# Optimization experiments

Measured on AMD Instinct MI355X. Metric: run time of the kernel, lower is better.

Reference implementation:

```python
import jax, jax.numpy as jnp
import numpy as np

B, N, C, H = 4, 2048, 768, 12
D = C // H  # 64
EPS = 1e-12


def setup_inputs() -> dict:
    key = jax.random.key(0)
    ks = jax.random.split(key, 8)
    s = 0.02
    return {
        "x": jax.random.normal(ks[0], (B, N, C), dtype=jnp.float32),
        "Wq": jax.random.normal(ks[1], (C, C), dtype=jnp.float32) * s,
        "bq": jnp.zeros((C,), dtype=jnp.float32),
        "Wkv": jax.random.normal(ks[2], (C, 2 * C), dtype=jnp.float32) * s,
        "bkv": jnp.zeros((2 * C,), dtype=jnp.float32),
        "Wproj": jax.random.normal(ks[3], (C, C), dtype=jnp.float32) * s,
        "bproj": jnp.zeros((C,), dtype=jnp.float32),
        "scale": jnp.full((1, H, 1, 1), D ** -0.5, dtype=jnp.float32),
    }


def _l2norm(t):
    # F.normalize(dim=-1): x / max(||x||_2, eps)
    n = jnp.sqrt(jnp.sum(t * t, axis=-1, keepdims=True))
    return t / jnp.maximum(n, EPS)


def reference(x, Wq, bq, Wkv, bkv, Wproj, bproj, scale):
    b, n, c = x.shape
    q = (x @ Wq + bq).reshape(b, n, H, D).transpose(0, 2, 1, 3)        # [B,H,N,D]
    kv = (x @ Wkv + bkv).reshape(b, n, 2, H, D).transpose(2, 0, 3, 1, 4)
    k, v = kv[0], kv[1]                                                # [B,H,N,D]
    q = _l2norm(q)
    k = _l2norm(k)
    attn = jnp.einsum("bhqd,bhkd->bhqk", q, k) * scale                 # [B,H,N,N]
    attn = jax.nn.softmax(attn, axis=-1)
    out = jnp.einsum("bhqk,bhkd->bhqd", attn, v)                       # [B,H,N,D]
    out = out.transpose(0, 2, 1, 3).reshape(b, n, c)
    return out @ Wproj + bproj
```

## Files before the change

### kernel.cpp

```cpp
#include <hip/hip_runtime.h>
#include <hip/hip_bf16.h>
#include <math.h>


typedef short bf16x8 __attribute__((ext_vector_type(8)));
typedef float f32x4 __attribute__((ext_vector_type(4)));
typedef float f32x16 __attribute__((ext_vector_type(16)));

static __device__ __forceinline__ unsigned short f2bf(float f) {
    unsigned int u = __float_as_uint(f);
    unsigned int r = u + 0x7fff + ((u >> 16) & 1);
    return (unsigned short)(r >> 16);
}
static __device__ __forceinline__ unsigned int pack2(float a, float b) {
    return (unsigned int)f2bf(a) | ((unsigned int)f2bf(b) << 16);
}
static __device__ __forceinline__ unsigned int cvtpk(float a, float b) {
    unsigned int r;
    asm("v_cvt_pk_bf16_f32 %0, %1, %2" : "=v"(r) : "v"(a), "v"(b));
    return r;
}
static __device__ __forceinline__ void gl_lds16(const void* g, void* l) {
    __builtin_amdgcn_global_load_lds(
        (const __attribute__((address_space(1))) unsigned int*)g,
        (__attribute__((address_space(3))) unsigned int*)l, 16, 0, 0);
}

__global__ __launch_bounds__(256) void convx_kernel(
    const float* __restrict__ in, unsigned short* __restrict__ out)
{
    size_t i = ((size_t)blockIdx.x * 256 + threadIdx.x) * 8;
    float4 a = *(const float4*)&in[i];
    float4 b = *(const float4*)&in[i + 4];
    uint4 o = make_uint4(pack2(a.x, a.y), pack2(a.z, a.w), pack2(b.x, b.y), pack2(b.z, b.w));
    *(uint4*)&out[i] = o;
}

__global__ __launch_bounds__(256) void convT_kernel(
    const float* __restrict__ A, int ldA, const float* __restrict__ Bs, int ldB, int split,
    unsigned short* __restrict__ out)
{
    __shared__ char tb[8192];
    const int c0 = blockIdx.x * 64, k0 = blockIdx.y * 64;
    const int t = threadIdx.x;
    const int kl = t >> 2, cq = (t & 3) * 16;
    const float* src; int ld; int cbase;
    if (c0 < split) { src = A;  ld = ldA; cbase = c0; }
    else            { src = Bs; ld = ldB; cbase = c0 - split; }
    #pragma unroll
    for (int jj = 0; jj < 4; ++jj) {
        float4 v = *(const float4*)&src[(size_t)(k0 + kl) * ld + cbase + cq + jj * 4];
        float vv[4] = {v.x, v.y, v.z, v.w};
        #pragma unroll
        for (int je = 0; je < 4; ++je) {
            int c = cq + jj * 4 + je;
            *(unsigned short*)(tb + c * 128 + ((kl * 2) ^ ((c & 7) << 4))) = f2bf(vv[je]);
        }
    }
    __syncthreads();
    const int cl = t >> 2, u2 = (t & 3) * 2;
    uint4 r0 = *(const uint4*)(tb + cl * 128 + ((u2 ^ (cl & 7)) << 4));
    uint4 r1 = *(const uint4*)(tb + cl * 128 + (((u2 + 1) ^ (cl & 7)) << 4));
    size_t ob = (size_t)(c0 + cl) * 768 + k0 + (t & 3) * 16;
    *(uint4*)&out[ob] = r0;
    *(uint4*)&out[ob + 8] = r1;
}

__global__ __launch_bounds__(256) void qkv_gemm_kernel(
    const unsigned short* __restrict__ xb, const unsigned short* __restrict__ WT,
    const float* __restrict__ bq, const float* __restrict__ bkv,
    const float* __restrict__ scale,
    unsigned short* __restrict__ Qb, unsigned short* __restrict__ Kb,
    unsigned short* __restrict__ Vtb)
{
    __shared__ char lds[32768] __attribute__((aligned(16)));

    const int ct = blockIdx.x;
    const int row0 = blockIdx.y * 128;
    const int tid = threadIdx.x;
    const int w = tid >> 6, l = tid & 63;
    const int g = l >> 4, ln = l & 15;
    const int wr = w >> 1, wc = w & 1;
    const int col0 = ct * 128;

    const int srow = (w & 1) * 64 + (l >> 3);
    const int su = ((l & 7) ^ (l >> 3)) * 16;
    const char* s = (w < 2)
        ? (const char*)xb + (size_t)(row0 + srow) * 1536 + su
        : (const char*)WT + (size_t)(col0 + srow) * 1536 + su;
    char* dbase = lds + ((w >= 2) ? 16384 : 0) + (w & 1) * 8192;

    f32x4 acc[4][4];
    #pragma unroll
    for (int m = 0; m < 4; ++m)
        #pragma unroll
        for (int n = 0; n < 4; ++n) acc[m][n] = (f32x4){0.f, 0.f, 0.f, 0.f};

    const int arow = (wr * 64 + ln) * 128;
    const int brow = 16384 + (wc * 64 + ln) * 128;
    const int x0 = ((0 + g) ^ (ln & 7)) * 16;
    const int x1 = ((4 + g) ^ (ln & 7)) * 16;

    for (int ks = 0; ks < 12; ++ks) {
        __syncthreads();
        #pragma unroll
        for (int j = 0; j < 8; ++j)
            gl_lds16(s + (size_t)j * 8 * 1536, dbase + j * 1024);
        s += 128;
        __syncthreads();
        #pragma unroll
        for (int kc = 0; kc < 2; ++kc) {
            const int xo = kc ? x1 : x0;
            bf16x8 af[4], bfr[4];
            #pragma unroll
            for (int m = 0; m < 4; ++m) af[m] = *(const bf16x8*)(lds + arow + m * 2048 + xo);
            #pragma unroll
            for (int n = 0; n < 4; ++n) bfr[n] = *(const bf16x8*)(lds + brow + n * 2048 + xo);
            #pragma unroll
            for (int m = 0; m < 4; ++m)
                #pragma unroll
                for (int n = 0; n < 4; ++n)
                    acc[m][n] = __builtin_amdgcn_mfma_f32_16x16x32_bf16(af[m], bfr[n], acc[m][n], 0, 0, 0);
        }
    }

    const int co = col0 + wc * 64 + ln;
    float bv[4];
    #pragma unroll
    for (int n = 0; n < 4; ++n) {
        int c = co + n * 16;
        bv[n] = (c < 768) ? bq[c] : bkv[c - 768];
    }
    const int region = ct / 6;
    const int h = (ct % 6) * 2 + wc;

    if (region < 2) {
        unsigned short* dst = (region == 0) ? Qb : Kb;
        const float post = (region == 0) ? scale[0] * 1.4426950408889634f : 1.0f;
        #pragma unroll
        for (int m = 0; m < 4; ++m) {
            #pragma unroll
            for (int n = 0; n < 4; ++n)
                #pragma unroll
                for (int r = 0; r < 4; ++r) acc[m][n][r] += bv[n];
            #pragma unroll
            for (int r = 0; r < 4; ++r) {
                float ss = 0.f;
                #pragma unroll
                for (int n = 0; n < 4; ++n) ss += acc[m][n][r] * acc[m][n][r];
                ss += __shfl_xor(ss, 1); ss += __shfl_xor(ss, 2);
                ss += __shfl_xor(ss, 4); ss += __shfl_xor(ss, 8);
                float inv = post / fmaxf(sqrtf(ss), 1e-12f);
                int t = row0 + wr * 64 + m * 16 + g * 4 + r;
                int b = t >> 11, nt = t & 2047;
                size_t base = ((size_t)(b * 12 + h) * 2048 + nt) * 64 + ln;
                #pragma unroll
                for (int n = 0; n < 4; ++n)
                    dst[base + n * 16] = f2bf(acc[m][n][r] * inv);
            }
        }
    } else {
        char* tb = lds + w * 8192;
        __syncthreads();
        #pragma unroll
        for (int m = 0; m < 4; ++m)
            #pragma unroll
            for (int n = 0; n < 4; ++n)
                #pragma unroll
                for (int r = 0; r < 4; ++r) {
                    int d = n * 16 + ln;
                    int tok = m * 16 + g * 4 + r;
                    *(unsigned short*)(tb + d * 128 + ((tok * 2) ^ ((d & 7) << 4))) =
                        f2bf(acc[m][n][r] + bv[n]);
                }
        __syncthreads();
        const int t0 = row0 + wr * 64;
        const int b = t0 >> 11, n0 = t0 & 2047;
        #pragma unroll
        for (int i = 0; i < 8; ++i) {
            int d = i * 8 + (l >> 3);
            uint4 v = *(const uint4*)(tb + d * 128 + (((l & 7) ^ (d & 7)) << 4));
            *(uint4*)&Vtb[((size_t)(b * 12 + h) * 64 + d) * 2048 + n0 + (l & 7) * 8] = v;
        }
    }
}

__global__ __launch_bounds__(256, 3) void attn_kernel(
    const unsigned short* __restrict__ Qg, const unsigned short* __restrict__ Kg,
    const unsigned short* __restrict__ Vtg,
    unsigned short* __restrict__ O)
{
    __shared__ char lds[32768] __attribute__((aligned(16)));

    const int bid = blockIdx.y * 16 + blockIdx.x;
    const int swzb = (bid & 7) * 96 + (bid >> 3);
    const int bh = swzb >> 4;
    const int q0 = (swzb & 15) * 128;

    const int tid = threadIdx.x;
    const int w  = tid >> 6;
    const int l  = tid & 63;
    const int lo = l & 31;
    const int hi = l >> 5;

    const int srow = w * 16 + (l >> 3);
    const int su   = ((l & 7) ^ (l >> 3)) * 16;
    const char* kS = (const char*)Kg  + ((size_t)bh * 2048 + srow) * 128 + su;
    const char* vS = (const char*)Vtg + ((size_t)bh * 64   + srow) * 4096 + su;
    char* kD = lds + w * 2048;
    char* vD = lds + 16384 + w * 2048;

    bf16x8 qf[4];
    {
        const unsigned short* qp = Qg + ((size_t)bh * 2048 + q0 + w * 32 + lo) * 64 + hi * 8;
        qf[0] = *(const bf16x8*)(qp);
        qf[1] = *(const bf16x8*)(qp + 16);
        qf[2] = *(const bf16x8*)(qp + 32);
        qf[3] = *(const bf16x8*)(qp + 48);
    }

    const int swz = (lo & 7) << 4;
    const int rowb = lo * 128;
    int coff[4];
    #pragma unroll
    for (int c = 0; c < 4; ++c) coff[c] = (c * 32 + hi * 16) ^ swz;

    f32x16 oacc0, oacc1;
    #pragma unroll
    for (int r = 0; r < 16; ++r) { oacc0[r] = 0.f; oacc1[r] = 0.f; }
    float rs = 0.f;

    const f32x16 zero16 = {0.f,0.f,0.f,0.f,0.f,0.f,0.f,0.f,0.f,0.f,0.f,0.f,0.f,0.f,0.f,0.f};

    auto compute = [&](const int OFF) {
        const char* Kb = lds + OFF;
        const char* Vb = lds + 16384 + OFF;

        f32x16 s0, s1;
        __builtin_amdgcn_s_setprio(1);
        s0 = __builtin_amdgcn_mfma_f32_32x32x16_bf16(*(const bf16x8*)(Kb + rowb + coff[0]), qf[0], zero16, 0, 0, 0);
        s0 = __builtin_amdgcn_mfma_f32_32x32x16_bf16(*(const bf16x8*)(Kb + rowb + coff[1]), qf[1], s0, 0, 0, 0);
        s0 = __builtin_amdgcn_mfma_f32_32x32x16_bf16(*(const bf16x8*)(Kb + rowb + coff[2]), qf[2], s0, 0, 0, 0);
        s0 = __builtin_amdgcn_mfma_f32_32x32x16_bf16(*(const bf16x8*)(Kb + rowb + coff[3]), qf[3], s0, 0, 0, 0);
        s1 = __builtin_amdgcn_mfma_f32_32x32x16_bf16(*(const bf16x8*)(Kb + 4096 + rowb + coff[0]), qf[0], zero16, 0, 0, 0);
        s1 = __builtin_amdgcn_mfma_f32_32x32x16_bf16(*(const bf16x8*)(Kb + 4096 + rowb + coff[1]), qf[1], s1, 0, 0, 0);
        s1 = __builtin_amdgcn_mfma_f32_32x32x16_bf16(*(const bf16x8*)(Kb + 4096 + rowb + coff[2]), qf[2], s1, 0, 0, 0);
        s1 = __builtin_amdgcn_mfma_f32_32x32x16_bf16(*(const bf16x8*)(Kb + 4096 + rowb + coff[3]), qf[3], s1, 0, 0, 0);
        __builtin_amdgcn_s_setprio(0);

        #pragma unroll
        for (int r = 0; r < 16; ++r) s0[r] = __builtin_amdgcn_exp2f(s0[r]);
        #pragma unroll
        for (int r = 0; r < 16; ++r) s1[r] = __builtin_amdgcn_exp2f(s1[r]);
        float t0 = 0.f, t1 = 0.f;
        #pragma unroll
        for (int r = 0; r < 16; ++r) { t0 += s0[r]; t1 += s1[r]; }
        rs += t0 + t1;

        #pragma unroll
        for (int kb = 0; kb < 2; ++kb) {
            const f32x16 ec = kb ? s1 : s0;
            #pragma unroll
            for (int ksb = 0; ksb < 2; ++ksb) {
                const int ks = kb * 2 + ksb;
                const int rqA = ksb * 2, rqB = rqA + 1;
                unsigned int uA0 = cvtpk(ec[rqA * 4 + 0], ec[rqA * 4 + 1]);
                unsigned int uA1 = cvtpk(ec[rqA * 4 + 2], ec[rqA * 4 + 3]);
                unsigned int uB0 = cvtpk(ec[rqB * 4 + 0], ec[rqB * 4 + 1]);
                unsigned int uB1 = cvtpk(ec[rqB * 4 + 2], ec[rqB * 4 + 3]);
                asm("v_permlane32_swap_b32 %0, %1" : "+v"(uA0), "+v"(uB0));
                asm("v_permlane32_swap_b32 %0, %1" : "+v"(uA1), "+v"(uB1));
                unsigned int fw[4] = {uA0, uA1, uB0, uB1};
                bf16x8 pa;
                __builtin_memcpy(&pa, fw, 16);
                __builtin_amdgcn_s_setprio(1);
                bf16x8 v0 = *(const bf16x8*)(Vb + rowb + coff[ks]);
                bf16x8 v1 = *(const bf16x8*)(Vb + 4096 + rowb + coff[ks]);
                oacc0 = __builtin_amdgcn_mfma_f32_32x32x16_bf16(pa, v0, oacc0, 0, 0, 0);
                oacc1 = __builtin_amdgcn_mfma_f32_32x32x16_bf16(pa, v1, oacc1, 0, 0, 0);
                __builtin_amdgcn_s_setprio(0);
            }
        }
    };

    gl_lds16(kS, kD);          gl_lds16(kS + 1024, kD + 1024);
    gl_lds16(vS, vD);          gl_lds16(vS + 32768, vD + 1024);
    kS += 8192; vS += 128;
    __syncthreads();

    #pragma unroll 1
    for (int it = 0; it < 16; ++it) {
        gl_lds16(kS, kD + 8192);          gl_lds16(kS + 1024, kD + 9216);
        gl_lds16(vS, vD + 8192);          gl_lds16(vS + 32768, vD + 9216);
        kS += 8192; vS += 128;
        compute(0);
        __syncthreads();
        if (it < 15) {
            gl_lds16(kS, kD);          gl_lds16(kS + 1024, kD + 1024);
            gl_lds16(vS, vD);          gl_lds16(vS + 32768, vD + 1024);
            kS += 8192; vS += 128;
        }
        compute(8192);
        __syncthreads();
    }

    float rsv = rs;
    rsv += __shfl_xor(rsv, 32);
    const int b = bh / 12, h = bh % 12;
    #pragma unroll
    for (int r = 0; r < 16; ++r) {
        const int qr = (r & 3) + 8 * (r >> 2) + 4 * hi;
        float inv = 1.0f / __shfl(rsv, qr);
        size_t base = ((size_t)(b * 2048 + q0 + w * 32 + qr)) * 768 + h * 64 + lo;
        O[base]      = f2bf(oacc0[r] * inv);
        O[base + 32] = f2bf(oacc1[r] * inv);
    }
}

__global__ __launch_bounds__(256) void proj_gemm_kernel(
    const unsigned short* __restrict__ Ob, const unsigned short* __restrict__ WT,
    const float* __restrict__ bp, float* __restrict__ out)
{
    __shared__ char lds[32768] __attribute__((aligned(16)));

    const int row0 = blockIdx.y * 128;
    const int col0 = blockIdx.x * 128;
    const int tid = threadIdx.x;
    const int w = tid >> 6, l = tid & 63;
    const int g = l >> 4, ln = l & 15;
    const int wr = w >> 1, wc = w & 1;

    const int srow = (w & 1) * 64 + (l >> 3);
    const int su = ((l & 7) ^ (l >> 3)) * 16;
    const char* s = (w < 2)
        ? (const char*)Ob + (size_t)(row0 + srow) * 1536 + su
        : (const char*)WT + (size_t)(col0 + srow) * 1536 + su;
    char* dbase = lds + ((w >= 2) ? 16384 : 0) + (w & 1) * 8192;

    f32x4 acc[4][4];
    #pragma unroll
    for (int m = 0; m < 4; ++m)
        #pragma unroll
        for (int n = 0; n < 4; ++n) acc[m][n] = (f32x4){0.f, 0.f, 0.f, 0.f};

    const int arow = (wr * 64 + ln) * 128;
    const int brow = 16384 + (wc * 64 + ln) * 128;
    const int x0 = ((0 + g) ^ (ln & 7)) * 16;
    const int x1 = ((4 + g) ^ (ln & 7)) * 16;

    for (int ks = 0; ks < 12; ++ks) {
        __syncthreads();
        #pragma unroll
        for (int j = 0; j < 8; ++j)
            gl_lds16(s + (size_t)j * 8 * 1536, dbase + j * 1024);
        s += 128;
        __syncthreads();
        #pragma unroll
        for (int kc = 0; kc < 2; ++kc) {
            const int xo = kc ? x1 : x0;
            bf16x8 af[4], bfr[4];
            #pragma unroll
            for (int m = 0; m < 4; ++m) af[m] = *(const bf16x8*)(lds + arow + m * 2048 + xo);
            #pragma unroll
            for (int n = 0; n < 4; ++n) bfr[n] = *(const bf16x8*)(lds + brow + n * 2048 + xo);
            #pragma unroll
            for (int m = 0; m < 4; ++m)
                #pragma unroll
                for (int n = 0; n < 4; ++n)
                    acc[m][n] = __builtin_amdgcn_mfma_f32_16x16x32_bf16(af[m], bfr[n], acc[m][n], 0, 0, 0);
        }
    }

    const int co = col0 + wc * 64 + ln;
    float bv[4];
    #pragma unroll
    for (int n = 0; n < 4; ++n) bv[n] = bp[co + n * 16];
    #pragma unroll
    for (int m = 0; m < 4; ++m)
        #pragma unroll
        for (int r = 0; r < 4; ++r) {
            int t = row0 + wr * 64 + m * 16 + g * 4 + r;
            #pragma unroll
            for (int n = 0; n < 4; ++n)
                out[(size_t)t * 768 + co + n * 16] = acc[m][n][r] + bv[n];
        }
}

extern "C" void kernel_launch(void* const* d_in, const int* in_sizes, int n_in,
                              void* d_out, int out_size, void* d_ws, size_t ws_size,
                              hipStream_t stream) {
    const float* x     = (const float*)d_in[0];
    const float* Wq    = (const float*)d_in[1];
    const float* bq    = (const float*)d_in[2];
    const float* Wkv   = (const float*)d_in[3];
    const float* bkv   = (const float*)d_in[4];
    const float* Wp    = (const float*)d_in[5];
    const float* bp    = (const float*)d_in[6];
    const float* scale = (const float*)d_in[7];
    float* out = (float*)d_out;

    unsigned short* ws = (unsigned short*)d_ws;
    const size_t SZ = (size_t)4 * 12 * 2048 * 64;
    unsigned short* xbw   = ws;
    unsigned short* WqkvT = xbw + SZ;
    unsigned short* WprjT = WqkvT + (size_t)2304 * 768;
    unsigned short* Qw    = WprjT + (size_t)768 * 768;
    unsigned short* Kw    = Qw + SZ;
    unsigned short* Vtw   = Kw + SZ;
    unsigned short* Ow    = Vtw + SZ;

    convx_kernel<<<3072, 256, 0, stream>>>(x, xbw);
    convT_kernel<<<dim3(36, 12), 256, 0, stream>>>(Wq, 768, Wkv, 1536, 768, WqkvT);
    convT_kernel<<<dim3(12, 12), 256, 0, stream>>>(Wp, 768, Wp, 768, 768, WprjT);
    qkv_gemm_kernel<<<dim3(18, 64), 256, 0, stream>>>(xbw, WqkvT, bq, bkv, scale, Qw, Kw, Vtw);
    attn_kernel<<<dim3(16, 48), 256, 0, stream>>>(Qw, Kw, Vtw, Ow);
    proj_gemm_kernel<<<dim3(6, 64), 256, 0, stream>>>(Ow, WprjT, bp, out);
}
```

Baseline: 145.1 us.

## Triple-buffer K/V in LDS and software-pipeline QK with PV across tiles

```diff
diff --git a/kernel.cpp b/kernel.cpp
--- a/kernel.cpp
+++ b/kernel.cpp
@@ -190,7 +190,7 @@
     const unsigned short* __restrict__ Vtg,
     unsigned short* __restrict__ O)
 {
-    __shared__ char lds[32768] __attribute__((aligned(16)));
+    __shared__ char lds[49152] __attribute__((aligned(16)));
 
     const int bid = blockIdx.y * 16 + blockIdx.x;
     const int swzb = (bid & 7) * 96 + (bid >> 3);
@@ -207,8 +207,21 @@
     const int su   = ((l & 7) ^ (l >> 3)) * 16;
     const char* kS = (const char*)Kg  + ((size_t)bh * 2048 + srow) * 128 + su;
     const char* vS = (const char*)Vtg + ((size_t)bh * 64   + srow) * 4096 + su;
-    char* kD = lds + w * 2048;
-    char* vD = lds + 16384 + w * 2048;
+    char* kD0 = lds + w * 2048;
+    char* vD0 = lds + 24576 + w * 2048;
+
+    auto stageK = [&](int t, int s) {
+        const char* p = kS + (size_t)t * 8192;
+        char* d = kD0 + s * 8192;
+        gl_lds16(p, d); gl_lds16(p + 1024, d + 1024);
+    };
+    auto stageV = [&](int t, int s) {
+        const char* p = vS + (size_t)t * 128;
+        char* d = vD0 + s * 8192;
+        gl_lds16(p, d); gl_lds16(p + 32768, d + 1024);
+    };
+
+    stageK(0, 0); stageV(0, 0); stageK(1, 1); stageV(1, 1); stageK(2, 2);
 
     bf16x8 qf[4];
     {
@@ -229,14 +242,12 @@
     #pragma unroll
     for (int r = 0; r < 16; ++r) { oacc0[r] = 0.f; oacc1[r] = 0.f; }
     float rs = 0.f;
+    unsigned int pcur[16];
 
     const f32x16 zero16 = {0.f,0.f,0.f,0.f,0.f,0.f,0.f,0.f,0.f,0.f,0.f,0.f,0.f,0.f,0.f,0.f};
 
-    auto compute = [&](const int OFF) {
-        const char* Kb = lds + OFF;
-        const char* Vb = lds + 16384 + OFF;
-
-        f32x16 s0, s1;
+    auto qk = [&](int slot, f32x16& s0, f32x16& s1) {
+        const char* Kb = lds + slot * 8192;
         __builtin_amdgcn_s_setprio(1);
         s0 = __builtin_amdgcn_mfma_f32_32x32x16_bf16(*(const bf16x8*)(Kb + rowb + coff[0]), qf[0], zero16, 0, 0, 0);
         s0 = __builtin_amdgcn_mfma_f32_32x32x16_bf16(*(const bf16x8*)(Kb + rowb + coff[1]), qf[1], s0, 0, 0, 0);
@@ -247,35 +258,48 @@
         s1 = __builtin_amdgcn_mfma_f32_32x32x16_bf16(*(const bf16x8*)(Kb + 4096 + rowb + coff[2]), qf[2], s1, 0, 0, 0);
         s1 = __builtin_amdgcn_mfma_f32_32x32x16_bf16(*(const bf16x8*)(Kb + 4096 + rowb + coff[3]), qf[3], s1, 0, 0, 0);
         __builtin_amdgcn_s_setprio(0);
-
-        #pragma unroll
-        for (int r = 0; r < 16; ++r) s0[r] = __builtin_amdgcn_exp2f(s0[r]);
-        #pragma unroll
-        for (int r = 0; r < 16; ++r) s1[r] = __builtin_amdgcn_exp2f(s1[r]);
-        float t0 = 0.f, t1 = 0.f;
-        #pragma unroll
-        for (int r = 0; r < 16; ++r) { t0 += s0[r]; t1 += s1[r]; }
-        rs += t0 + t1;
-
+    };
+
+    auto exppack = [&](const f32x16& s0, const f32x16& s1) {
         #pragma unroll
         for (int kb = 0; kb < 2; ++kb) {
-            const f32x16 ec = kb ? s1 : s0;
+            float e[16];
+            #pragma unroll
+            for (int r = 0; r < 16; ++r)
+                e[r] = __builtin_amdgcn_exp2f(kb ? s1[r] : s0[r]);
+            float t = 0.f;
+            #pragma unroll
+            for (int r = 0; r < 16; r += 4) t += (e[r] + e[r+1]) + (e[r+2] + e[r+3]);
+            rs += t;
             #pragma unroll
             for (int ksb = 0; ksb < 2; ++ksb) {
-                const int ks = kb * 2 + ksb;
-                const int rqA = ksb * 2, rqB = rqA + 1;
-                unsigned int uA0 = cvtpk(ec[rqA * 4 + 0], ec[rqA * 4 + 1]);
-                unsigned int uA1 = cvtpk(ec[rqA * 4 + 2], ec[rqA * 4 + 3]);
-                unsigned int uB0 = cvtpk(ec[rqB * 4 + 0], ec[rqB * 4 + 1]);
-                unsigned int uB1 = cvtpk(ec[rqB * 4 + 2], ec[rqB * 4 + 3]);
+                pcur[kb*8 + ksb*4 + 0] = cvtpk(e[ksb*8 + 0], e[ksb*8 + 1]);
+                pcur[kb*8 + ksb*4 + 1] = cvtpk(e[ksb*8 + 2], e[ksb*8 + 3]);
+                pcur[kb*8 + ksb*4 + 2] = cvtpk(e[ksb*8 + 4], e[ksb*8 + 5]);
+                pcur[kb*8 + ksb*4 + 3] = cvtpk(e[ksb*8 + 6], e[ksb*8 + 7]);
+            }
+        }
+    };
+
+    auto pv = [&](int slot) {
+        const char* Vb = lds + 24576 + slot * 8192;
+        #pragma unroll
+        for (int kb = 0; kb < 2; ++kb) {
+            #pragma unroll
+            for (int ksb = 0; ksb < 2; ++ksb) {
+                const int base = kb*8 + ksb*4;
+                unsigned int uA0 = pcur[base + 0];
+                unsigned int uA1 = pcur[base + 1];
+                unsigned int uB0 = pcur[base + 2];
+                unsigned int uB1 = pcur[base + 3];
                 asm("v_permlane32_swap_b32 %0, %1" : "+v"(uA0), "+v"(uB0));
                 asm("v_permlane32_swap_b32 %0, %1" : "+v"(uA1), "+v"(uB1));
                 unsigned int fw[4] = {uA0, uA1, uB0, uB1};
                 bf16x8 pa;
                 __builtin_memcpy(&pa, fw, 16);
                 __builtin_amdgcn_s_setprio(1);
-                bf16x8 v0 = *(const bf16x8*)(Vb + rowb + coff[ks]);
-                bf16x8 v1 = *(const bf16x8*)(Vb + 4096 + rowb + coff[ks]);
+                bf16x8 v0 = *(const bf16x8*)(Vb + rowb + coff[kb*2 + ksb]);
+                bf16x8 v1 = *(const bf16x8*)(Vb + 4096 + rowb + coff[kb*2 + ksb]);
                 oacc0 = __builtin_amdgcn_mfma_f32_32x32x16_bf16(pa, v0, oacc0, 0, 0, 0);
                 oacc1 = __builtin_amdgcn_mfma_f32_32x32x16_bf16(pa, v1, oacc1, 0, 0, 0);
                 __builtin_amdgcn_s_setprio(0);
@@ -283,26 +307,35 @@
         }
     };
 
-    gl_lds16(kS, kD);          gl_lds16(kS + 1024, kD + 1024);
-    gl_lds16(vS, vD);          gl_lds16(vS + 32768, vD + 1024);
-    kS += 8192; vS += 128;
-    __syncthreads();
+    asm volatile("s_waitcnt vmcnt(6)" ::: "memory");
+    __builtin_amdgcn_s_barrier();
+    {
+        f32x16 t0, t1;
+        qk(0, t0, t1);
+        exppack(t0, t1);
+    }
+
+    auto half = [&](int j, int skr, int svr, int svs, bool stK, bool stV, bool doQK, int vm) {
+        if (vm == 4)      asm volatile("s_waitcnt vmcnt(4)" ::: "memory");
+        else if (vm == 2) asm volatile("s_waitcnt vmcnt(2)" ::: "memory");
+        else              asm volatile("s_waitcnt vmcnt(0)" ::: "memory");
+        __builtin_amdgcn_s_barrier();
+        if (stK) stageK(j + 3, svr);
+        if (stV) stageV(j + 2, svs);
+        f32x16 t0, t1;
+        if (doQK) qk(skr, t0, t1);
+        pv(svr);
+        if (doQK) exppack(t0, t1);
+    };
 
     #pragma unroll 1
-    for (int it = 0; it < 16; ++it) {
-        gl_lds16(kS, kD + 8192);          gl_lds16(kS + 1024, kD + 9216);
-        gl_lds16(vS, vD + 8192);          gl_lds16(vS + 32768, vD + 9216);
-        kS += 8192; vS += 128;
-        compute(0);
-        __syncthreads();
-        if (it < 15) {
-            gl_lds16(kS, kD);          gl_lds16(kS + 1024, kD + 1024);
-            gl_lds16(vS, vD);          gl_lds16(vS + 32768, vD + 1024);
-            kS += 8192; vS += 128;
-        }
-        compute(8192);
-        __syncthreads();
-    }
+    for (int jj = 0; jj < 30; jj += 3) {
+        half(jj,     1, 0, 2, jj     <= 28, true, true, 4);
+        half(jj + 1, 2, 1, 0, jj + 1 <= 28, true, true, 4);
+        half(jj + 2, 0, 2, 1, jj + 2 <= 28, true, true, 4);
+    }
+    half(30, 1, 0, 0, false, false, true,  2);
+    half(31, 0, 1, 0, false, false, false, 0);
 
     float rsv = rs;
     rsv += __shfl_xor(rsv, 32);
```

Result: no change. 144.3 us (-0.6%).

## Halve attention block to two waves each computing 64 query rows; merge weight conversion launches

Applied to the files above, without the earlier changes.

```diff
diff --git a/kernel.cpp b/kernel.cpp
--- a/kernel.cpp
+++ b/kernel.cpp
@@ -37,16 +37,21 @@
 }
 
 __global__ __launch_bounds__(256) void convT_kernel(
-    const float* __restrict__ A, int ldA, const float* __restrict__ Bs, int ldB, int split,
-    unsigned short* __restrict__ out)
+    const float* __restrict__ Wq, const float* __restrict__ Wkv, const float* __restrict__ Wp,
+    unsigned short* __restrict__ WqkvT, unsigned short* __restrict__ WprjT)
 {
     __shared__ char tb[8192];
-    const int c0 = blockIdx.x * 64, k0 = blockIdx.y * 64;
+    const int bx = blockIdx.x, k0 = blockIdx.y * 64;
+    const float* src; int ld; int cbase; unsigned short* out; int c0;
+    if (bx < 36) {
+        c0 = bx * 64; out = WqkvT;
+        if (c0 < 768) { src = Wq;  ld = 768;  cbase = c0; }
+        else          { src = Wkv; ld = 1536; cbase = c0 - 768; }
+    } else {
+        c0 = (bx - 36) * 64; out = WprjT; src = Wp; ld = 768; cbase = c0;
+    }
     const int t = threadIdx.x;
     const int kl = t >> 2, cq = (t & 3) * 16;
-    const float* src; int ld; int cbase;
-    if (c0 < split) { src = A;  ld = ldA; cbase = c0; }
-    else            { src = Bs; ld = ldB; cbase = c0 - split; }
     #pragma unroll
     for (int jj = 0; jj < 4; ++jj) {
         float4 v = *(const float4*)&src[(size_t)(k0 + kl) * ld + cbase + cq + jj * 4];
@@ -185,7 +190,7 @@
     }
 }
 
-__global__ __launch_bounds__(256, 3) void attn_kernel(
+__global__ __launch_bounds__(128, 2) void attn_kernel(
     const unsigned short* __restrict__ Qg, const unsigned short* __restrict__ Kg,
     const unsigned short* __restrict__ Vtg,
     unsigned short* __restrict__ O)
@@ -203,20 +208,33 @@
     const int lo = l & 31;
     const int hi = l >> 5;
 
-    const int srow = w * 16 + (l >> 3);
+    const int srow = w * 32 + (l >> 3);
     const int su   = ((l & 7) ^ (l >> 3)) * 16;
     const char* kS = (const char*)Kg  + ((size_t)bh * 2048 + srow) * 128 + su;
     const char* vS = (const char*)Vtg + ((size_t)bh * 64   + srow) * 4096 + su;
-    char* kD = lds + w * 2048;
-    char* vD = lds + 16384 + w * 2048;
-
-    bf16x8 qf[4];
+    char* kD = lds + w * 4096;
+    char* vD = lds + 16384 + w * 4096;
+
+    auto stage = [&](int t, int buf) {
+        const char* pk = kS + (size_t)t * 8192;
+        const char* pv = vS + (size_t)t * 128;
+        char* dk = kD + buf * 8192;
+        char* dv = vD + buf * 8192;
+        #pragma unroll
+        for (int i = 0; i < 4; ++i) {
+            gl_lds16(pk + i * 1024, dk + i * 1024);
+            gl_lds16(pv + (size_t)i * 32768, dv + i * 1024);
+        }
+    };
+
+    bf16x8 qfA[4], qfB[4];
     {
-        const unsigned short* qp = Qg + ((size_t)bh * 2048 + q0 + w * 32 + lo) * 64 + hi * 8;
-        qf[0] = *(const bf16x8*)(qp);
-        qf[1] = *(const bf16x8*)(qp + 16);
-        qf[2] = *(const bf16x8*)(qp + 32);
-        qf[3] = *(const bf16x8*)(qp + 48);
+        const unsigned short* qp = Qg + ((size_t)bh * 2048 + q0 + w * 64 + lo) * 64 + hi * 8;
+        #pragma unroll
+        for (int c = 0; c < 4; ++c) {
+            qfA[c] = *(const bf16x8*)(qp + c * 16);
+            qfB[c] = *(const bf16x8*)(qp + 2048 + c * 16);
+        }
     }
 
     const int swz = (lo & 7) << 4;
@@ -225,10 +243,10 @@
     #pragma unroll
     for (int c = 0; c < 4; ++c) coff[c] = (c * 32 + hi * 16) ^ swz;
 
-    f32x16 oacc0, oacc1;
-    #pragma unroll
-    for (int r = 0; r < 16; ++r) { oacc0[r] = 0.f; oacc1[r] = 0.f; }
-    float rs = 0.f;
+    f32x16 oA0, oA1, oB0, oB1;
+    #pragma unroll
+    for (int r = 0; r < 16; ++r) { oA0[r] = 0.f; oA1[r] = 0.f; oB0[r] = 0.f; oB1[r] = 0.f; }
+    float rsA = 0.f, rsB = 0.f;
 
     const f32x16 zero16 = {0.f,0.f,0.f,0.f,0.f,0.f,0.f,0.f,0.f,0.f,0.f,0.f,0.f,0.f,0.f,0.f};
 
@@ -236,84 +254,126 @@
         const char* Kb = lds + OFF;
         const char* Vb = lds + 16384 + OFF;
 
-        f32x16 s0, s1;
+        bf16x8 kf[4], kg2[4];
+        #pragma unroll
+        for (int c = 0; c < 4; ++c) {
+            kf[c]  = *(const bf16x8*)(Kb + rowb + coff[c]);
+            kg2[c] = *(const bf16x8*)(Kb + 4096 + rowb + coff[c]);
+        }
+
+        f32x16 sA0, sA1, sB0, sB1;
         __builtin_amdgcn_s_setprio(1);
-        s0 = __builtin_amdgcn_mfma_f32_32x32x16_bf16(*(const bf16x8*)(Kb + rowb + coff[0]), qf[0], zero16, 0, 0, 0);
-        s0 = __builtin_amdgcn_mfma_f32_32x32x16_bf16(*(const bf16x8*)(Kb + rowb + coff[1]), qf[1], s0, 0, 0, 0);
-        s0 = __builtin_amdgcn_mfma_f32_32x32x16_bf16(*(const bf16x8*)(Kb + rowb + coff[2]), qf[2], s0, 0, 0, 0);
-        s0 = __builtin_amdgcn_mfma_f32_32x32x16_bf16(*(const bf16x8*)(Kb + rowb + coff[3]), qf[3], s0, 0, 0, 0);
-        s1 = __builtin_amdgcn_mfma_f32_32x32x16_bf16(*(const bf16x8*)(Kb + 4096 + rowb + coff[0]), qf[0], zero16, 0, 0, 0);
-        s1 = __builtin_amdgcn_mfma_f32_32x32x16_bf16(*(const bf16x8*)(Kb + 4096 + rowb + coff[1]), qf[1], s1, 0, 0, 0);
-        s1 = __builtin_amdgcn_mfma_f32_32x32x16_bf16(*(const bf16x8*)(Kb + 4096 + rowb + coff[2]), qf[2], s1, 0, 0, 0);
-        s1 = __builtin_amdgcn_mfma_f32_32x32x16_bf16(*(const bf16x8*)(Kb + 4096 + rowb + coff[3]), qf[3], s1, 0, 0, 0);
+        sA0 = __builtin_amdgcn_mfma_f32_32x32x16_bf16(kf[0], qfA[0], zero16, 0, 0, 0);
+        sA0 = __builtin_amdgcn_mfma_f32_32x32x16_bf16(kf[1], qfA[1], sA0, 0, 0, 0);
+        sA0 = __builtin_amdgcn_mfma_f32_32x32x16_bf16(kf[2], qfA[2], sA0, 0, 0, 0);
+        sA0 = __builtin_amdgcn_mfma_f32_32x32x16_bf16(kf[3], qfA[3], sA0, 0, 0, 0);
+        sA1 = __builtin_amdgcn_mfma_f32_32x32x16_bf16(kg2[0], qfA[0], zero16, 0, 0, 0);
+        sA1 = __builtin_amdgcn_mfma_f32_32x32x16_bf16(kg2[1], qfA[1], sA1, 0, 0, 0);
+        sA1 = __builtin_amdgcn_mfma_f32_32x32x16_bf16(kg2[2], qfA[2], sA1, 0, 0, 0);
+        sA1 = __builtin_amdgcn_mfma_f32_32x32x16_bf16(kg2[3], qfA[3], sA1, 0, 0, 0);
+        sB0 = __builtin_amdgcn_mfma_f32_32x32x16_bf16(kf[0], qfB[0], zero16, 0, 0, 0);
+        sB0 = __builtin_amdgcn_mfma_f32_32x32x16_bf16(kf[1], qfB[1], sB0, 0, 0, 0);
+        sB0 = __builtin_amdgcn_mfma_f32_32x32x16_bf16(kf[2], qfB[2], sB0, 0, 0, 0);
+        sB0 = __builtin_amdgcn_mfma_f32_32x32x16_bf16(kf[3], qfB[3], sB0, 0, 0, 0);
+        sB1 = __builtin_amdgcn_mfma_f32_32x32x16_bf16(kg2[0], qfB[0], zero16, 0, 0, 0);
+        sB1 = __builtin_amdgcn_mfma_f32_32x32x16_bf16(kg2[1], qfB[1], sB1, 0, 0, 0);
+        sB1 = __builtin_amdgcn_mfma_f32_32x32x16_bf16(kg2[2], qfB[2], sB1, 0, 0, 0);
+        sB1 = __builtin_amdgcn_mfma_f32_32x32x16_bf16(kg2[3], qfB[3], sB1, 0, 0, 0);
         __builtin_amdgcn_s_setprio(0);
 
-        #pragma unroll
-        for (int r = 0; r < 16; ++r) s0[r] = __builtin_amdgcn_exp2f(s0[r]);
-        #pragma unroll
-        for (int r = 0; r < 16; ++r) s1[r] = __builtin_amdgcn_exp2f(s1[r]);
-        float t0 = 0.f, t1 = 0.f;
-        #pragma unroll
-        for (int r = 0; r < 16; ++r) { t0 += s0[r]; t1 += s1[r]; }
-        rs += t0 + t1;
-
+        unsigned int pA[16], pB[16];
         #pragma unroll
         for (int kb = 0; kb < 2; ++kb) {
-            const f32x16 ec = kb ? s1 : s0;
+            float e[16];
+            #pragma unroll
+            for (int r = 0; r < 16; ++r)
+                e[r] = __builtin_amdgcn_exp2f(kb ? sA1[r] : sA0[r]);
+            float t = 0.f;
+            #pragma unroll
+            for (int r = 0; r < 16; r += 4) t += (e[r] + e[r+1]) + (e[r+2] + e[r+3]);
+            rsA += t;
             #pragma unroll
             for (int ksb = 0; ksb < 2; ++ksb) {
-                const int ks = kb * 2 + ksb;
-                const int rqA = ksb * 2, rqB = rqA + 1;
-                unsigned int uA0 = cvtpk(ec[rqA * 4 + 0], ec[rqA * 4 + 1]);
-                unsigned int uA1 = cvtpk(ec[rqA * 4 + 2], ec[rqA * 4 + 3]);
-                unsigned int uB0 = cvtpk(ec[rqB * 4 + 0], ec[rqB * 4 + 1]);
-                unsigned int uB1 = cvtpk(ec[rqB * 4 + 2], ec[rqB * 4 + 3]);
-                asm("v_permlane32_swap_b32 %0, %1" : "+v"(uA0), "+v"(uB0));
-                asm("v_permlane32_swap_b32 %0, %1" : "+v"(uA1), "+v"(uB1));
-                unsigned int fw[4] = {uA0, uA1, uB0, uB1};
-                bf16x8 pa;
-                __builtin_memcpy(&pa, fw, 16);
-                __builtin_amdgcn_s_setprio(1);
+                pA[kb*8 + ksb*4 + 0] = cvtpk(e[ksb*8 + 0], e[ksb*8 + 1]);
+                pA[kb*8 + ksb*4 + 1] = cvtpk(e[ksb*8 + 2], e[ksb*8 + 3]);
+                pA[kb*8 + ksb*4 + 2] = cvtpk(e[ksb*8 + 4], e[ksb*8 + 5]);
+                pA[kb*8 + ksb*4 + 3] = cvtpk(e[ksb*8 + 6], e[ksb*8 + 7]);
+            }
+        }
+        #pragma unroll
+        for (int kb = 0; kb < 2; ++kb) {
+            float e[16];
+            #pragma unroll
+            for (int r = 0; r < 16; ++r)
+                e[r] = __builtin_amdgcn_exp2f(kb ? sB1[r] : sB0[r]);
+            float t = 0.f;
+            #pragma unroll
+            for (int r = 0; r < 16; r += 4) t += (e[r] + e[r+1]) + (e[r+2] + e[r+3]);
+            rsB += t;
+            #pragma unroll
+            for (int ksb = 0; ksb < 2; ++ksb) {
+                pB[kb*8 + ksb*4 + 0] = cvtpk(e[ksb*8 + 0], e[ksb*8 + 1]);
+                pB[kb*8 + ksb*4 + 1] = cvtpk(e[ksb*8 + 2], e[ksb*8 + 3]);
+                pB[kb*8 + ksb*4 + 2] = cvtpk(e[ksb*8 + 4], e[ksb*8 + 5]);
+                pB[kb*8 + ksb*4 + 3] = cvtpk(e[ksb*8 + 6], e[ksb*8 + 7]);
+            }
+        }
+
+        #pragma unroll
+        for (int kb = 0; kb < 2; ++kb) {
+            #pragma unroll
+            for (int ksb = 0; ksb < 2; ++ksb) {
+                const int base = kb*8 + ksb*4;
+                const int ks = kb*2 + ksb;
                 bf16x8 v0 = *(const bf16x8*)(Vb + rowb + coff[ks]);
                 bf16x8 v1 = *(const bf16x8*)(Vb + 4096 + rowb + coff[ks]);
-                oacc0 = __builtin_amdgcn_mfma_f32_32x32x16_bf16(pa, v0, oacc0, 0, 0, 0);
-                oacc1 = __builtin_amdgcn_mfma_f32_32x32x16_bf16(pa, v1, oacc1, 0, 0, 0);
+                unsigned int a0 = pA[base], a1 = pA[base+1], a2 = pA[base+2], a3 = pA[base+3];
+                asm("v_permlane32_swap_b32 %0, %1" : "+v"(a0), "+v"(a2));
+                asm("v_permlane32_swap_b32 %0, %1" : "+v"(a1), "+v"(a3));
+                unsigned int fwA[4] = {a0, a1, a2, a3};
+                bf16x8 paA; __builtin_memcpy(&paA, fwA, 16);
+                unsigned int b0 = pB[base], b1 = pB[base+1], b2 = pB[base+2], b3 = pB[base+3];
+                asm("v_permlane32_swap_b32 %0, %1" : "+v"(b0), "+v"(b2));
+                asm("v_permlane32_swap_b32 %0, %1" : "+v"(b1), "+v"(b3));
+                unsigned int fwB[4] = {b0, b1, b2, b3};
+                bf16x8 paB; __builtin_memcpy(&paB, fwB, 16);
+                __builtin_amdgcn_s_setprio(1);
+                oA0 = __builtin_amdgcn_mfma_f32_32x32x16_bf16(paA, v0, oA0, 0, 0, 0);
+                oA1 = __builtin_amdgcn_mfma_f32_32x32x16_bf16(paA, v1, oA1, 0, 0, 0);
+                oB0 = __builtin_amdgcn_mfma_f32_32x32x16_bf16(paB, v0, oB0, 0, 0, 0);
+                oB1 = __builtin_amdgcn_mfma_f32_32x32x16_bf16(paB, v1, oB1, 0, 0, 0);
                 __builtin_amdgcn_s_setprio(0);
             }
         }
     };
 
-    gl_lds16(kS, kD);          gl_lds16(kS + 1024, kD + 1024);
-    gl_lds16(vS, vD);          gl_lds16(vS + 32768, vD + 1024);
-    kS += 8192; vS += 128;
+    stage(0, 0);
     __syncthreads();
 
     #pragma unroll 1
     for (int it = 0; it < 16; ++it) {
-        gl_lds16(kS, kD + 8192);          gl_lds16(kS + 1024, kD + 9216);
-        gl_lds16(vS, vD + 8192);          gl_lds16(vS + 32768, vD + 9216);
-        kS += 8192; vS += 128;
+        stage(2 * it + 1, 1);
         compute(0);
         __syncthreads();
-        if (it < 15) {
-            gl_lds16(kS, kD);          gl_lds16(kS + 1024, kD + 1024);
-            gl_lds16(vS, vD);          gl_lds16(vS + 32768, vD + 1024);
-            kS += 8192; vS += 128;
-        }
+        if (it < 15) stage(2 * it + 2, 0);
         compute(8192);
         __syncthreads();
     }
 
-    float rsv = rs;
-    rsv += __shfl_xor(rsv, 32);
+    float vA = rsA; vA += __shfl_xor(vA, 32);
+    float vB = rsB; vB += __shfl_xor(vB, 32);
     const int b = bh / 12, h = bh % 12;
     #pragma unroll
     for (int r = 0; r < 16; ++r) {
         const int qr = (r & 3) + 8 * (r >> 2) + 4 * hi;
-        float inv = 1.0f / __shfl(rsv, qr);
-        size_t base = ((size_t)(b * 2048 + q0 + w * 32 + qr)) * 768 + h * 64 + lo;
-        O[base]      = f2bf(oacc0[r] * inv);
-        O[base + 32] = f2bf(oacc1[r] * inv);
+        float invA = 1.0f / __shfl(vA, qr);
+        float invB = 1.0f / __shfl(vB, qr);
+        size_t baseA = ((size_t)(b * 2048 + q0 + w * 64 + qr)) * 768 + h * 64 + lo;
+        O[baseA]      = f2bf(oA0[r] * invA);
+        O[baseA + 32] = f2bf(oA1[r] * invA);
+        size_t baseB = baseA + (size_t)32 * 768;
+        O[baseB]      = f2bf(oB0[r] * invB);
+        O[baseB + 32] = f2bf(oB1[r] * invB);
     }
 }
 
@@ -410,9 +470,8 @@
     unsigned short* Ow    = Vtw + SZ;
 
     convx_kernel<<<3072, 256, 0, stream>>>(x, xbw);
-    convT_kernel<<<dim3(36, 12), 256, 0, stream>>>(Wq, 768, Wkv, 1536, 768, WqkvT);
-    convT_kernel<<<dim3(12, 12), 256, 0, stream>>>(Wp, 768, Wp, 768, 768, WprjT);
+    convT_kernel<<<dim3(48, 12), 256, 0, stream>>>(Wq, Wkv, Wp, WqkvT, WprjT);
     qkv_gemm_kernel<<<dim3(18, 64), 256, 0, stream>>>(xbw, WqkvT, bq, bkv, scale, Qw, Kw, Vtw);
-    attn_kernel<<<dim3(16, 48), 256, 0, stream>>>(Qw, Kw, Vtw, Ow);
+    attn_kernel<<<dim3(16, 48), 128, 0, stream>>>(Qw, Kw, Vtw, Ow);
     proj_gemm_kernel<<<dim3(6, 64), 256, 0, stream>>>(Ow, WprjT, bp, out);
 }
```

New measurement: 148.5 us. +2.3%, slower.

## Stage attention K/V through registers with padded LDS and merge weight transposes

Applied to the files above, without the earlier changes.

```diff
diff --git a/kernel.cpp b/kernel.cpp
--- a/kernel.cpp
+++ b/kernel.cpp
@@ -37,16 +37,21 @@
 }
 
 __global__ __launch_bounds__(256) void convT_kernel(
-    const float* __restrict__ A, int ldA, const float* __restrict__ Bs, int ldB, int split,
-    unsigned short* __restrict__ out)
+    const float* __restrict__ Wq, const float* __restrict__ Wkv, const float* __restrict__ Wp,
+    unsigned short* __restrict__ WqkvT, unsigned short* __restrict__ WprjT)
 {
     __shared__ char tb[8192];
-    const int c0 = blockIdx.x * 64, k0 = blockIdx.y * 64;
+    const int bx = blockIdx.x, k0 = blockIdx.y * 64;
+    const float* src; int ld; int cbase; unsigned short* out; int c0;
+    if (bx < 36) {
+        c0 = bx * 64; out = WqkvT;
+        if (c0 < 768) { src = Wq;  ld = 768;  cbase = c0; }
+        else          { src = Wkv; ld = 1536; cbase = c0 - 768; }
+    } else {
+        c0 = (bx - 36) * 64; out = WprjT; src = Wp; ld = 768; cbase = c0;
+    }
     const int t = threadIdx.x;
     const int kl = t >> 2, cq = (t & 3) * 16;
-    const float* src; int ld; int cbase;
-    if (c0 < split) { src = A;  ld = ldA; cbase = c0; }
-    else            { src = Bs; ld = ldB; cbase = c0 - split; }
     #pragma unroll
     for (int jj = 0; jj < 4; ++jj) {
         float4 v = *(const float4*)&src[(size_t)(k0 + kl) * ld + cbase + cq + jj * 4];
@@ -190,7 +195,7 @@
     const unsigned short* __restrict__ Vtg,
     unsigned short* __restrict__ O)
 {
-    __shared__ char lds[32768] __attribute__((aligned(16)));
+    __shared__ char lds[33792] __attribute__((aligned(16)));
 
     const int bid = blockIdx.y * 16 + blockIdx.x;
     const int swzb = (bid & 7) * 96 + (bid >> 3);
@@ -204,11 +209,26 @@
     const int hi = l >> 5;
 
     const int srow = w * 16 + (l >> 3);
-    const int su   = ((l & 7) ^ (l >> 3)) * 16;
-    const char* kS = (const char*)Kg  + ((size_t)bh * 2048 + srow) * 128 + su;
-    const char* vS = (const char*)Vtg + ((size_t)bh * 64   + srow) * 4096 + su;
-    char* kD = lds + w * 2048;
-    char* vD = lds + 16384 + w * 2048;
+    const int scol = (l & 7) * 16;
+    const char* kG = (const char*)Kg  + ((size_t)bh * 2048 + srow) * 128 + scol;
+    const char* vG = (const char*)Vtg + ((size_t)bh * 64   + srow) * 4096 + scol;
+    const int wOff = srow * 132 + scol;
+
+    uint4 kr0, kr1, vr0, vr1;
+    auto issue = [&](int t) {
+        const char* kp = kG + (size_t)t * 8192;
+        const char* vp = vG + (size_t)t * 128;
+        kr0 = *(const uint4*)(kp);
+        kr1 = *(const uint4*)(kp + 1024);
+        vr0 = *(const uint4*)(vp);
+        vr1 = *(const uint4*)(vp + 32768);
+    };
+    auto writeb = [&](int buf) {
+        char* kb = lds + buf * 8448 + wOff;
+        char* vb = lds + 16896 + buf * 8448 + wOff;
+        *(uint4*)kb = kr0; *(uint4*)(kb + 1056) = kr1;
+        *(uint4*)vb = vr0; *(uint4*)(vb + 1056) = vr1;
+    };
 
     bf16x8 qf[4];
     {
@@ -219,11 +239,10 @@
         qf[3] = *(const bf16x8*)(qp + 48);
     }
 
-    const int swz = (lo & 7) << 4;
-    const int rowb = lo * 128;
+    const int rowb = lo * 132;
     int coff[4];
     #pragma unroll
-    for (int c = 0; c < 4; ++c) coff[c] = (c * 32 + hi * 16) ^ swz;
+    for (int c = 0; c < 4; ++c) coff[c] = c * 32 + hi * 16;
 
     f32x16 oacc0, oacc1;
     #pragma unroll
@@ -234,7 +253,7 @@
 
     auto compute = [&](const int OFF) {
         const char* Kb = lds + OFF;
-        const char* Vb = lds + 16384 + OFF;
+        const char* Vb = lds + 16896 + OFF;
 
         f32x16 s0, s1;
         __builtin_amdgcn_s_setprio(1);
@@ -242,32 +261,42 @@
         s0 = __builtin_amdgcn_mfma_f32_32x32x16_bf16(*(const bf16x8*)(Kb + rowb + coff[1]), qf[1], s0, 0, 0, 0);
         s0 = __builtin_amdgcn_mfma_f32_32x32x16_bf16(*(const bf16x8*)(Kb + rowb + coff[2]), qf[2], s0, 0, 0, 0);
         s0 = __builtin_amdgcn_mfma_f32_32x32x16_bf16(*(const bf16x8*)(Kb + rowb + coff[3]), qf[3], s0, 0, 0, 0);
-        s1 = __builtin_amdgcn_mfma_f32_32x32x16_bf16(*(const bf16x8*)(Kb + 4096 + rowb + coff[0]), qf[0], zero16, 0, 0, 0);
-        s1 = __builtin_amdgcn_mfma_f32_32x32x16_bf16(*(const bf16x8*)(Kb + 4096 + rowb + coff[1]), qf[1], s1, 0, 0, 0);
-        s1 = __builtin_amdgcn_mfma_f32_32x32x16_bf16(*(const bf16x8*)(Kb + 4096 + rowb + coff[2]), qf[2], s1, 0, 0, 0);
-        s1 = __builtin_amdgcn_mfma_f32_32x32x16_bf16(*(const bf16x8*)(Kb + 4096 + rowb + coff[3]), qf[3], s1, 0, 0, 0);
+        s1 = __builtin_amdgcn_mfma_f32_32x32x16_bf16(*(const bf16x8*)(Kb + 4224 + rowb + coff[0]), qf[0], zero16, 0, 0, 0);
+        s1 = __builtin_amdgcn_mfma_f32_32x32x16_bf16(*(const bf16x8*)(Kb + 4224 + rowb + coff[1]), qf[1], s1, 0, 0, 0);
+        s1 = __builtin_amdgcn_mfma_f32_32x32x16_bf16(*(const bf16x8*)(Kb + 4224 + rowb + coff[2]), qf[2], s1, 0, 0, 0);
+        s1 = __builtin_amdgcn_mfma_f32_32x32x16_bf16(*(const bf16x8*)(Kb + 4224 + rowb + coff[3]), qf[3], s1, 0, 0, 0);
         __builtin_amdgcn_s_setprio(0);
 
-        #pragma unroll
-        for (int r = 0; r < 16; ++r) s0[r] = __builtin_amdgcn_exp2f(s0[r]);
-        #pragma unroll
-        for (int r = 0; r < 16; ++r) s1[r] = __builtin_amdgcn_exp2f(s1[r]);
-        float t0 = 0.f, t1 = 0.f;
-        #pragma unroll
-        for (int r = 0; r < 16; ++r) { t0 += s0[r]; t1 += s1[r]; }
-        rs += t0 + t1;
-
+        unsigned int pcur[16];
         #pragma unroll
         for (int kb = 0; kb < 2; ++kb) {
-            const f32x16 ec = kb ? s1 : s0;
+            float e[16];
+            #pragma unroll
+            for (int r = 0; r < 16; ++r)
+                e[r] = __builtin_amdgcn_exp2f(kb ? s1[r] : s0[r]);
+            float t = 0.f;
+            #pragma unroll
+            for (int r = 0; r < 16; r += 4) t += (e[r] + e[r+1]) + (e[r+2] + e[r+3]);
+            rs += t;
             #pragma unroll
             for (int ksb = 0; ksb < 2; ++ksb) {
-                const int ks = kb * 2 + ksb;
-                const int rqA = ksb * 2, rqB = rqA + 1;
-                unsigned int uA0 = cvtpk(ec[rqA * 4 + 0], ec[rqA * 4 + 1]);
-                unsigned int uA1 = cvtpk(ec[rqA * 4 + 2], ec[rqA * 4 + 3]);
-                unsigned int uB0 = cvtpk(ec[rqB * 4 + 0], ec[rqB * 4 + 1]);
-                unsigned int uB1 = cvtpk(ec[rqB * 4 + 2], ec[rqB * 4 + 3]);
+                pcur[kb*8 + ksb*4 + 0] = cvtpk(e[ksb*8 + 0], e[ksb*8 + 1]);
+                pcur[kb*8 + ksb*4 + 1] = cvtpk(e[ksb*8 + 2], e[ksb*8 + 3]);
+                pcur[kb*8 + ksb*4 + 2] = cvtpk(e[ksb*8 + 4], e[ksb*8 + 5]);
+                pcur[kb*8 + ksb*4 + 3] = cvtpk(e[ksb*8 + 6], e[ksb*8 + 7]);
+            }
+        }
+
+        #pragma unroll
+        for (int kb = 0; kb < 2; ++kb) {
+            #pragma unroll
+            for (int ksb = 0; ksb < 2; ++ksb) {
+                const int base = kb*8 + ksb*4;
+                const int ks = kb*2 + ksb;
+                unsigned int uA0 = pcur[base + 0];
+                unsigned int uA1 = pcur[base + 1];
+                unsigned int uB0 = pcur[base + 2];
+                unsigned int uB1 = pcur[base + 3];
                 asm("v_permlane32_swap_b32 %0, %1" : "+v"(uA0), "+v"(uB0));
                 asm("v_permlane32_swap_b32 %0, %1" : "+v"(uA1), "+v"(uB1));
                 unsigned int fw[4] = {uA0, uA1, uB0, uB1};
@@ -275,7 +304,7 @@
                 __builtin_memcpy(&pa, fw, 16);
                 __builtin_amdgcn_s_setprio(1);
                 bf16x8 v0 = *(const bf16x8*)(Vb + rowb + coff[ks]);
-                bf16x8 v1 = *(const bf16x8*)(Vb + 4096 + rowb + coff[ks]);
+                bf16x8 v1 = *(const bf16x8*)(Vb + 4224 + rowb + coff[ks]);
                 oacc0 = __builtin_amdgcn_mfma_f32_32x32x16_bf16(pa, v0, oacc0, 0, 0, 0);
                 oacc1 = __builtin_amdgcn_mfma_f32_32x32x16_bf16(pa, v1, oacc1, 0, 0, 0);
                 __builtin_amdgcn_s_setprio(0);
@@ -283,24 +312,18 @@
         }
     };
 
-    gl_lds16(kS, kD);          gl_lds16(kS + 1024, kD + 1024);
-    gl_lds16(vS, vD);          gl_lds16(vS + 32768, vD + 1024);
-    kS += 8192; vS += 128;
+    issue(0); writeb(0);
     __syncthreads();
 
     #pragma unroll 1
     for (int it = 0; it < 16; ++it) {
-        gl_lds16(kS, kD + 8192);          gl_lds16(kS + 1024, kD + 9216);
-        gl_lds16(vS, vD + 8192);          gl_lds16(vS + 32768, vD + 9216);
-        kS += 8192; vS += 128;
+        issue(2 * it + 1);
         compute(0);
-        __syncthreads();
-        if (it < 15) {
-            gl_lds16(kS, kD);          gl_lds16(kS + 1024, kD + 1024);
-            gl_lds16(vS, vD);          gl_lds16(vS + 32768, vD + 1024);
-            kS += 8192; vS += 128;
-        }
-        compute(8192);
+        writeb(1);
+        __syncthreads();
+        if (it < 15) issue(2 * it + 2);
+        compute(8448);
+        if (it < 15) writeb(0);
         __syncthreads();
     }
 
@@ -410,8 +433,7 @@
     unsigned short* Ow    = Vtw + SZ;
 
     convx_kernel<<<3072, 256, 0, stream>>>(x, xbw);
-    convT_kernel<<<dim3(36, 12), 256, 0, stream>>>(Wq, 768, Wkv, 1536, 768, WqkvT);
-    convT_kernel<<<dim3(12, 12), 256, 0, stream>>>(Wp, 768, Wp, 768, 768, WprjT);
+    convT_kernel<<<dim3(48, 12), 256, 0, stream>>>(Wq, Wkv, Wp, WqkvT, WprjT);
     qkv_gemm_kernel<<<dim3(18, 64), 256, 0, stream>>>(xbw, WqkvT, bq, bkv, scale, Qw, Kw, Vtw);
     attn_kernel<<<dim3(16, 48), 256, 0, stream>>>(Qw, Kw, Vtw, Ow);
     proj_gemm_kernel<<<dim3(6, 64), 256, 0, stream>>>(Ow, WprjT, bp, out);
```

Result: slower. 286.2 us (+97.2%).
